# Kernel tuning notes

Hardware: AMD Instinct MI355X
Metric: run time of the kernel (lower is better)

Reference implementation:

```python
import jax, jax.numpy as jnp
import numpy as np
import math

B, H, L = 8, 512, 4096
N2 = 32  # d_state // 2


def setup_inputs() -> dict:
    key = jax.random.key(0)
    ks = jax.random.split(key, 8)
    u = jax.random.normal(ks[0], (B, H, L), dtype=jnp.float32)
    C = jax.random.normal(ks[1], (H, N2, 2), dtype=jnp.float32)  # view_as_real of cfloat C
    # log_dt ~ Uniform[log(dt_min), log(dt_max)], dt_min=1e-3, dt_max=0.1
    log_dt = jax.random.uniform(ks[2], (H,), dtype=jnp.float32,
                                minval=math.log(0.001), maxval=math.log(0.1))
    log_A_real = jnp.log(0.5 * jnp.ones((H, N2), dtype=jnp.float32))
    A_imag = math.pi * jnp.broadcast_to(jnp.arange(N2, dtype=jnp.float32), (H, N2))
    D = jax.random.normal(ks[3], (H,), dtype=jnp.float32)
    # pointwise Conv1d(H, 2H, kernel_size=1): weight (2H, H), bias (2H)
    fan = 1.0 / math.sqrt(H)
    W = jax.random.uniform(ks[4], (2 * H, H), dtype=jnp.float32, minval=-fan, maxval=fan)
    b = jax.random.uniform(ks[5], (2 * H,), dtype=jnp.float32, minval=-fan, maxval=fan)
    return {"u": u, "C": C, "log_dt": log_dt, "log_A_real": log_A_real,
            "A_imag": A_imag, "D": D, "W": W, "b": b}


def reference(u, C, log_dt, log_A_real, A_imag, D, W, b):
    Lb = u.shape[-1]
    # --- S4DKernel: kernel k of shape (H, L) ---
    dt = jnp.exp(log_dt)                                  # (H,)
    Cc = C[..., 0] + 1j * C[..., 1]                       # (H, N2) complex
    A = -jnp.exp(log_A_real) + 1j * A_imag                # (H, N2)
    dtA = A * dt[:, None]                                 # (H, N2)
    # Vandermonde: exp(dtA * l) for l in [0, L)
    K = jnp.exp(dtA[:, :, None] * jnp.arange(Lb, dtype=jnp.float32))  # (H, N2, L)
    Cmod = Cc * (jnp.exp(dtA) - 1.0) / A                  # (H, N2)
    k = 2.0 * jnp.einsum('hn,hnl->hl', Cmod, K).real      # (H, L)
    # --- FFT convolution (length 2L, causal) ---
    n = 2 * Lb
    k_f = jnp.fft.rfft(k, n=n)                            # (H, L+1)
    u_f = jnp.fft.rfft(u, n=n)                            # (B, H, L+1)
    y = jnp.fft.irfft(u_f * k_f, n=n)[..., :Lb]           # (B, H, L)
    # skip connection
    y = y + u * D[:, None]
    # activation (torch nn.GELU default = exact erf form)
    y = jax.nn.gelu(y, approximate=False)
    # pointwise conv (H -> 2H) + GLU over channel dim
    y = jnp.einsum('oh,bhl->bol', W, y) + b[None, :, None]  # (B, 2H, L)
    a, g = jnp.split(y, 2, axis=1)
    return a * jax.nn.sigmoid(g)                          # (B, H, L)
```

## Files before the change

### kernel.cpp

```cpp
#include <hip/hip_runtime.h>
#include <hip/hip_bf16.h>

constexpr int Bn = 8, Hn = 512, Ln = 4096, N2n = 32;

typedef _Float16 f16;
typedef __attribute__((ext_vector_type(8))) _Float16 f16x8;
typedef __attribute__((ext_vector_type(4))) _Float16 f16x4;
typedef __attribute__((ext_vector_type(2))) _Float16 f16x2;
typedef __attribute__((ext_vector_type(4))) float f32x4;

typedef void __attribute__((address_space(1))) gvoid;
typedef void __attribute__((address_space(3))) lvoid;

__global__ __launch_bounds__(64) void k_mats1(
    const float* __restrict__ C, const float* __restrict__ log_dt,
    const float* __restrict__ logA, const float* __restrict__ Aim,
    f16* __restrict__ Vg, f16* __restrict__ A3g, float2* __restrict__ w64g) {
  __shared__ f16 VT[64 * 64];
  __shared__ f16 QT[64 * 64];
  __shared__ float kp[64][33];
  __shared__ float ks[64];
  const int h = blockIdx.x, tid = threadIdx.x, n = tid & 31;

  if (tid < 32) {
    const int idx = h * N2n + n;
    float dt = expf(log_dt[h]);
    float Ar = -expf(logA[idx]);
    float Ai = Aim[idx];
    float dr = Ar * dt, di = Ai * dt;
    float er = expf(dr);
    float wr = er * cosf(di), wi = er * sinf(di);
    float den = Ar * Ar + Ai * Ai;
    float e1r = wr - 1.0f, e1i = wi;
    float tr = (e1r * Ar + e1i * Ai) / den;
    float ti = (e1i * Ar - e1r * Ai) / den;
    float Cr = C[idx * 2 + 0], Ci = C[idx * 2 + 1];
    float c2r = 2.0f * (Cr * tr - Ci * ti);
    float c2i = 2.0f * (Cr * ti + Ci * tr);

    float wpr = 1.f, wpi = 0.f;
    for (int p = 0; p <= 64; ++p) {
      float cwr = c2r * wpr - c2i * wpi;
      float cwi = c2r * wpi + c2i * wpr;
      if (p < 64) {
        const int j = 63 - p, ch = j >> 3, jo = j & 7;
        const int s0 = 2 * n, s1 = 2 * n + 1;
        VT[s0 * 64 + ((ch ^ (s0 & 7)) * 8) + jo] = (f16)wpr;
        VT[s1 * 64 + ((ch ^ (s1 & 7)) * 8) + jo] = (f16)wpi;
        kp[p][n] = cwr;
      }
      if (p >= 1) {
        const int t = p - 1, c0 = 2 * n;
        const int ch = (c0 >> 3) ^ (t & 7);
        QT[t * 64 + ch * 8 + (c0 & 7)]     = (f16)cwr;
        QT[t * 64 + ch * 8 + (c0 & 7) + 1] = (f16)(-cwi);
      }
      if (p == 64) w64g[h * 32 + n] = make_float2(wpr, wpi);
      float nr = wpr * wr - wpi * wi;
      float ni = wpr * wi + wpi * wr;
      wpr = nr; wpi = ni;
    }
  }
  __syncthreads();
  float s = 0.f;
#pragma unroll
  for (int m = 0; m < 32; ++m) s += kp[tid][m];
  ks[tid] = s;
  __syncthreads();
  const int t = tid;
#pragma unroll
  for (int c = 0; c < 8; ++c) {
    f16x8 row;
#pragma unroll
    for (int jo = 0; jo < 8; ++jo) {
      int j = c * 8 + jo;
      row[jo] = (j <= t) ? (f16)ks[t - j] : (f16)0.f;
    }
    *(f16x8*)&A3g[(size_t)h * 8192 + t * 128 + ((c ^ (t & 7)) * 8)] = row;
  }
#pragma unroll
  for (int c = 0; c < 8; ++c)
    *(f16x8*)&Vg[(size_t)h * 4096 + tid * 64 + c * 8] = *(f16x8*)&VT[tid * 64 + c * 8];
#pragma unroll
  for (int c = 0; c < 8; ++c)
    *(f16x8*)&A3g[(size_t)h * 8192 + tid * 128 + 64 + c * 8] = *(f16x8*)&QT[tid * 64 + c * 8];
}

__global__ void conv_w(const float* __restrict__ W, f16* __restrict__ Wh) {
  int i = blockIdx.x * 256 + threadIdx.x;
  if (i < 2 * Hn * Hn) Wh[i] = (f16)W[i];
}

__global__ __launch_bounds__(256, 4) void s4d_mid(
    const float* __restrict__ u, const f16* __restrict__ Vg,
    const f16* __restrict__ A3g, const float2* __restrict__ w64g,
    const float* __restrict__ Dv, f16* __restrict__ yg) {
  __shared__ f16 MATS[8192];
  __shared__ f16 U[4096];
  __shared__ f16 LE[4096];
  __shared__ float2 Pbuf[4][32];
  const int tid = threadIdx.x, wid = tid >> 6, lane = tid & 63;
  const int h = ((blockIdx.x >> 6) << 3) | (blockIdx.x & 7);
  const int b = (blockIdx.x >> 3) & 7;
  const float Dh = Dv[h];

#pragma unroll
  for (int q = 0; q < 2; ++q)
    __builtin_amdgcn_global_load_lds((const gvoid*)(Vg + (size_t)h * 4096 + (q * 256 + tid) * 8),
                                     (lvoid*)&MATS[(q * 256 + wid * 64) * 8], 16, 0, 0);
#pragma unroll
  for (int i = 0; i < 4; ++i) {
    int e = (i * 256 + tid) * 4;
    float4 uv = *(const float4*)(u + ((size_t)(b * Hn + h)) * Ln + e);
    int col = e >> 6, j = e & 63;
    f16x4 hv = {(f16)uv.x, (f16)uv.y, (f16)uv.z, (f16)uv.w};
    *(f16x4*)&U[col * 64 + ((j >> 3) ^ (col & 7)) * 8 + (j & 7)] = hv;
  }
  asm volatile("s_waitcnt vmcnt(0)" ::: "memory");
  __syncthreads();

  const int col = wid * 16 + (lane & 15);
  f32x4 acc[4];
#pragma unroll
  for (int i = 0; i < 4; ++i) acc[i] = (f32x4){0.f, 0.f, 0.f, 0.f};
#pragma unroll
  for (int ks = 0; ks < 2; ++ks) {
    const int kc = ks * 4 + (lane >> 4);
    f16x8 bv = *(const f16x8*)&U[col * 64 + ((kc ^ (col & 7)) * 8)];
#pragma unroll
    for (int mf = 0; mf < 4; ++mf) {
      int row = mf * 16 + (lane & 15);
      f16x8 a = *(const f16x8*)&MATS[row * 64 + ((kc ^ (row & 7)) * 8)];
      acc[mf] = __builtin_amdgcn_mfma_f32_16x16x32_f16(a, bv, acc[mf], 0, 0, 0);
    }
  }
  __syncthreads();

#pragma unroll
  for (int q = 0; q < 4; ++q)
    __builtin_amdgcn_global_load_lds((const gvoid*)(A3g + (size_t)h * 8192 + (q * 256 + tid) * 8),
                                     (lvoid*)&MATS[(q * 256 + wid * 64) * 8], 16, 0, 0);

#pragma unroll
  for (int mf = 0; mf < 4; ++mf) {
    int st0 = mf * 16 + (lane >> 4) * 4;
    f16x4 o = {(f16)acc[mf][0], (f16)acc[mf][1], (f16)acc[mf][2], (f16)acc[mf][3]};
    *(f16x4*)&LE[col * 64 + (((st0 >> 3) ^ (col & 7)) << 3) + (st0 & 7)] = o;
  }
  __syncthreads();

  {
    const int n = lane & 31, q = wid;
    const float2 wT = w64g[h * 32 + n];
    float qr = wT.x, qi = wT.y;
#pragma unroll
    for (int s = 0; s < 4; ++s) {
      float nr = qr * qr - qi * qi;
      float ni = 2.f * qr * qi;
      qr = nr; qi = ni;
    }
    f16x2 Lb[16];
    float er = 0.f, ei = 0.f;
    if (lane < 32) {
#pragma unroll
      for (int k = 0; k < 16; ++k) {
        int blk = q * 16 + k;
        int fi = blk * 64 + (((n >> 2) ^ (blk & 7)) << 3) + ((n & 3) << 1);
        Lb[k] = *(const f16x2*)&LE[fi];
      }
#pragma unroll
      for (int k = 0; k < 16; ++k) {
        float nr = fmaf(wT.x, er, fmaf(-wT.y, ei, (float)Lb[k][0]));
        float ni = fmaf(wT.y, er, fmaf(wT.x, ei, (float)Lb[k][1]));
        er = nr; ei = ni;
      }
      Pbuf[q][n] = make_float2(er, ei);
    }
    __syncthreads();
    if (lane < 32) {
      float orr = 0.f, oii = 0.f;
      for (int p = 0; p < q; ++p) {
        float2 Pp = Pbuf[p][n];
        float nr = fmaf(qr, orr, fmaf(-qi, oii, Pp.x));
        float ni = fmaf(qi, orr, fmaf(qr, oii, Pp.y));
        orr = nr; oii = ni;
      }
      er = orr; ei = oii;
#pragma unroll
      for (int k = 0; k < 16; ++k) {
        int blk = q * 16 + k;
        int fi = blk * 64 + (((n >> 2) ^ (blk & 7)) << 3) + ((n & 3) << 1);
        *(f16x2*)&LE[fi] = (f16x2){(f16)er, (f16)ei};
        float nr = fmaf(wT.x, er, fmaf(-wT.y, ei, (float)Lb[k][0]));
        float ni = fmaf(wT.y, er, fmaf(wT.x, ei, (float)Lb[k][1]));
        er = nr; ei = ni;
      }
    }
  }
  asm volatile("s_waitcnt vmcnt(0)" ::: "memory");
  __syncthreads();

  f32x4 acc4[4];
#pragma unroll
  for (int i = 0; i < 4; ++i) acc4[i] = (f32x4){0.f, 0.f, 0.f, 0.f};
#pragma unroll
  for (int ks = 0; ks < 4; ++ks) {
    const int kc = ks * 4 + (lane >> 4);
    f16x8 bf;
    if (ks < 2) bf = *(const f16x8*)&U[col * 64 + ((kc ^ (col & 7)) << 3)];
    else        bf = *(const f16x8*)&LE[col * 64 + (((kc - 8) ^ (col & 7)) << 3)];
#pragma unroll
    for (int mf = 0; mf < 4; ++mf) {
      int row = mf * 16 + (lane & 15);
      f16x8 af = *(const f16x8*)&MATS[row * 128 + ((kc ^ (row & 7)) << 3)];
      acc4[mf] = __builtin_amdgcn_mfma_f32_16x16x32_f16(af, bf, acc4[mf], 0, 0, 0);
    }
  }
  const int t0 = (lane >> 4) * 4;
#pragma unroll
  for (int mf = 0; mf < 4; ++mf) {
    const int tb = mf * 16 + t0;
    f16x4 uq = *(const f16x4*)&U[col * 64 + (((tb >> 3) ^ (col & 7)) << 3) + (tb & 7)];
    f16x4 o;
#pragma unroll
    for (int r = 0; r < 4; ++r) {
      float v = acc4[mf][r] + Dh * (float)uq[r];
      float g2 = v * fmaf(0.0713548163f, v * v, 1.5957691216f);
      o[r] = (f16)(v * __builtin_amdgcn_rcpf(1.0f + __expf(-g2)));
    }
    *(f16x4*)&yg[((size_t)(b * Hn + h)) * Ln + col * 64 + tb] = o;
  }
}

__global__ __launch_bounds__(256) void k_transpose(
    const f16* __restrict__ yg, f16* __restrict__ gyT) {
  __shared__ float T[64][65];
  const int bid = blockIdx.x, tid = threadIdx.x;
  const int b = bid >> 9, hg = (bid >> 6) & 7, lg = bid & 63;
  const int h0 = hg * 64, l0 = lg * 64;
  const int hi = tid >> 2, lc = (tid & 3) * 16;
  const f16* src = yg + ((size_t)(b * Hn + h0 + hi)) * Ln + l0 + lc;
  f16x8 v0 = *(const f16x8*)src;
  f16x8 v1 = *(const f16x8*)(src + 8);
#pragma unroll
  for (int e = 0; e < 8; ++e) T[lc + e][hi] = (float)v0[e];
#pragma unroll
  for (int e = 0; e < 8; ++e) T[lc + 8 + e][hi] = (float)v1[e];
  __syncthreads();
  const int li = tid >> 2, hc = (tid & 3) * 16;
  f16x8 o0, o1;
#pragma unroll
  for (int e = 0; e < 8; ++e) o0[e] = (f16)T[li][hc + e];
#pragma unroll
  for (int e = 0; e < 8; ++e) o1[e] = (f16)T[li][hc + 8 + e];
  f16* dst = gyT + ((size_t)b * Ln + l0 + li) * Hn + h0 + hc;
  *(f16x8*)dst = o0;
  *(f16x8*)(dst + 8) = o1;
}

__global__ __launch_bounds__(512, 2) void s4d_gemm(
    const f16* __restrict__ Wh, const f16* __restrict__ gyT,
    const float* __restrict__ bias, float* __restrict__ out) {
  __shared__ f16 Asd[2][256 * 64];
  __shared__ f16 Bsd[2][256 * 64];
  __shared__ float biasS[256];
  const int tid = threadIdx.x;
  const int wid = tid >> 6, lane = tid & 63;
  const int nt = blockIdx.x & 127;
  const int mt = blockIdx.x >> 7;
  const int b = nt >> 4;
  const int l0 = (nt & 15) * 256;
  const int m0 = mt * 128;
  const int isG = wid >> 2;
  const int w4 = wid & 3;

  if (tid < 128) biasS[tid] = bias[m0 + tid];
  else if (tid < 256) biasS[tid] = bias[Hn + m0 + (tid - 128)];

  const int srow8 = lane >> 3;
  const int sp = lane & 7;

#define STAGE(BUF, KT)                                                                   \
  {                                                                                      \
    const int k0 = (KT) * 64;                                                            \
    _Pragma("unroll")                                                                    \
    for (int q = 0; q < 4; ++q) {                                                        \
      const int r = q * 64 + wid * 8 + srow8;                                \
      const int wr = (r < 128) ? (m0 + r) : (Hn + m0 + r - 128);                         \
      const f16* srcA = Wh + ((size_t)wr * 512 + k0 + ((sp ^ (r & 7)) * 8));             \
      __builtin_amdgcn_global_load_lds((const gvoid*)srcA,                               \
          (lvoid*)&Asd[BUF][(q * 64 + wid * 8) * 64], 16, 0, 0);                         \
    }                                                                                    \
    _Pragma("unroll")                                                                    \
    for (int q = 0; q < 4; ++q) {                                                        \
      const int r = q * 64 + wid * 8 + srow8;                          \
      const f16* srcB = gyT + (((size_t)b * Ln + l0 + r) * Hn + k0 + ((sp ^ (r & 7)) * 8)); \
      __builtin_amdgcn_global_load_lds((const gvoid*)srcB,                               \
          (lvoid*)&Bsd[BUF][(q * 64 + wid * 8) * 64], 16, 0, 0);                         \
    }                                                                                    \
  }

  f32x4 acc[8][4];
#pragma unroll
  for (int i = 0; i < 8; ++i)
#pragma unroll
    for (int j = 0; j < 4; ++j) acc[i][j] = (f32x4){0.f, 0.f, 0.f, 0.f};

  STAGE(0, 0);
  asm volatile("s_waitcnt vmcnt(0)" ::: "memory");
  __syncthreads();

  for (int kt = 0; kt < 8; ++kt) {
    const int cur = kt & 1;
    if (kt < 7) STAGE(cur ^ 1, kt + 1);
#pragma unroll
    for (int kk = 0; kk < 2; ++kk) {
      const int kc = kk * 4 + (lane >> 4);
      f16x8 bf[4];
#pragma unroll
      for (int nf = 0; nf < 4; ++nf) {
        const int cl = w4 * 64 + nf * 16 + (lane & 15);
        bf[nf] = *(const f16x8*)&Bsd[cur][cl * 64 + ((kc ^ (cl & 7)) * 8)];
      }
#pragma unroll
      for (int mf = 0; mf < 8; ++mf) {
        const int ra = isG * 128 + mf * 16 + (lane & 15);
        f16x8 af = *(const f16x8*)&Asd[cur][ra * 64 + ((kc ^ (ra & 7)) * 8)];
#pragma unroll
        for (int nf = 0; nf < 4; ++nf)
          acc[mf][nf] = __builtin_amdgcn_mfma_f32_16x16x32_f16(af, bf[nf], acc[mf][nf], 0, 0, 0);
      }
    }
    asm volatile("s_waitcnt vmcnt(0)" ::: "memory");
    __syncthreads();
  }

  f16* SIG = &Asd[0][0];
  const int slot = (w4 * 64 + lane) * 128;
  if (isG) {
#pragma unroll
    for (int mf = 0; mf < 8; ++mf) {
#pragma unroll
      for (int np = 0; np < 2; ++np) {
        f16x8 c;
#pragma unroll
        for (int e = 0; e < 8; ++e) {
          const int nf = np * 2 + (e >> 2), r = e & 3;
          const int rowh = mf * 16 + (lane >> 4) * 4 + r;
          float gv = acc[mf][nf][r] + biasS[128 + rowh];
          c[e] = (f16)__builtin_amdgcn_rcpf(1.0f + __expf(-gv));
        }
        const int cid = mf * 2 + np;
        *(f16x8*)&SIG[slot + ((cid ^ (lane & 15)) * 8)] = c;
      }
    }
  }
  __syncthreads();
  if (!isG) {
#pragma unroll
    for (int mf = 0; mf < 8; ++mf) {
#pragma unroll
      for (int np = 0; np < 2; ++np) {
        const int cid = mf * 2 + np;
        f16x8 sg = *(const f16x8*)&SIG[slot + ((cid ^ (lane & 15)) * 8)];
#pragma unroll
        for (int e = 0; e < 8; ++e) {
          const int nf = np * 2 + (e >> 2), r = e & 3;
          const int rowh = mf * 16 + (lane >> 4) * 4 + r;
          const int hh = m0 + rowh;
          const int l = l0 + w4 * 64 + nf * 16 + (lane & 15);
          float av = acc[mf][nf][r] + biasS[rowh];
          out[((size_t)b * Hn + hh) * Ln + l] = av * (float)sg[e];
        }
      }
    }
  }
#undef STAGE
}

extern "C" void kernel_launch(void* const* d_in, const int* in_sizes, int n_in,
                              void* d_out, int out_size, void* d_ws, size_t ws_size,
                              hipStream_t stream) {
  (void)in_sizes; (void)n_in; (void)out_size; (void)ws_size;
  const float* u     = (const float*)d_in[0];
  const float* C     = (const float*)d_in[1];
  const float* logdt = (const float*)d_in[2];
  const float* logA  = (const float*)d_in[3];
  const float* Aim   = (const float*)d_in[4];
  const float* Dv    = (const float*)d_in[5];
  const float* W     = (const float*)d_in[6];
  const float* bias  = (const float*)d_in[7];
  float* out = (float*)d_out;

  char* ws = (char*)d_ws;
  f16*    gyT  = (f16*)ws;
  f16*    Vg   = (f16*)(ws + (size_t)(32 << 20));
  f16*    A3g  = (f16*)(ws + (size_t)(36 << 20));
  float2* w64g = (float2*)(ws + (size_t)(44 << 20));
  f16*    Wh   = (f16*)(ws + (size_t)(45 << 20));
  f16*    yg   = (f16*)d_out;

  hipLaunchKernelGGL(k_mats1, dim3(Hn), dim3(64), 0, stream, C, logdt, logA, Aim, Vg, A3g, w64g);
  hipLaunchKernelGGL(conv_w, dim3(2048), dim3(256), 0, stream, W, Wh);
  hipLaunchKernelGGL(s4d_mid, dim3(Hn * Bn), dim3(256), 0, stream, u, Vg, A3g, w64g, Dv, yg);
  hipLaunchKernelGGL(k_transpose, dim3(Bn * 8 * 64), dim3(256), 0, stream, yg, gyT);
  hipLaunchKernelGGL(s4d_gemm, dim3(512), dim3(512), 0, stream, Wh, gyT, bias, out);
}
```

Baseline: 103.1 us.

## Pre-swizzle W into MFMA fragment order and load A operands directly

The weight conversion kernel now writes W in f16 already arranged in MFMA A-fragment order, using vectorized 8-wide stores. The GEMM drops the A shared-memory tile and has each lane load its fragments straight from global memory with contiguous 16-byte reads. This halves the LDS footprint and removes A staging and LDS reads, which could raise occupancy. The cost is that A loads are no longer prefetched through the double buffer, so global latency may show up in the inner loop.

After: 114.7 us. +11.3%, slower.

```diff
diff --git a/kernel.cpp b/kernel.cpp
--- a/kernel.cpp
+++ b/kernel.cpp
@@ -86,9 +86,21 @@
     *(f16x8*)&A3g[(size_t)h * 8192 + tid * 128 + 64 + c * 8] = *(f16x8*)&QT[tid * 64 + c * 8];
 }
 
-__global__ void conv_w(const float* __restrict__ W, f16* __restrict__ Wh) {
-  int i = blockIdx.x * 256 + threadIdx.x;
-  if (i < 2 * Hn * Hn) Wh[i] = (f16)W[i];
+__global__ void conv_w(const float* __restrict__ W, f16* __restrict__ WhF) {
+  int g = blockIdx.x * 256 + threadIdx.x;
+  int lane = g & 63;
+  int mf = (g >> 6) & 7;
+  int kk = (g >> 9) & 1;
+  int kt = (g >> 10) & 7;
+  int mt = (g >> 13) & 3;
+  int isG = (g >> 15) & 1;
+  int wr = isG * 512 + mt * 128 + mf * 16 + (lane & 15);
+  int k  = kt * 64 + kk * 32 + (lane >> 4) * 8;
+  const float4* src = (const float4*)(W + (size_t)wr * 512 + k);
+  float4 a = src[0], c = src[1];
+  f16x8 o = {(f16)a.x, (f16)a.y, (f16)a.z, (f16)a.w,
+             (f16)c.x, (f16)c.y, (f16)c.z, (f16)c.w};
+  *(f16x8*)&WhF[(size_t)g * 8] = o;
 }
 
 __global__ __launch_bounds__(256, 4) void s4d_mid(
@@ -259,9 +271,8 @@
 }
 
 __global__ __launch_bounds__(512, 2) void s4d_gemm(
-    const f16* __restrict__ Wh, const f16* __restrict__ gyT,
+    const f16* __restrict__ WhF, const f16* __restrict__ gyT,
     const float* __restrict__ bias, float* __restrict__ out) {
-  __shared__ f16 Asd[2][256 * 64];
   __shared__ f16 Bsd[2][256 * 64];
   __shared__ float biasS[256];
   const int tid = threadIdx.x;
@@ -280,24 +291,16 @@
   const int srow8 = lane >> 3;
   const int sp = lane & 7;
 
-#define STAGE(BUF, KT)                                                                   \
-  {                                                                                      \
-    const int k0 = (KT) * 64;                                                            \
-    _Pragma("unroll")                                                                    \
-    for (int q = 0; q < 4; ++q) {                                                        \
-      const int r = q * 64 + wid * 8 + srow8;                                \
-      const int wr = (r < 128) ? (m0 + r) : (Hn + m0 + r - 128);                         \
-      const f16* srcA = Wh + ((size_t)wr * 512 + k0 + ((sp ^ (r & 7)) * 8));             \
-      __builtin_amdgcn_global_load_lds((const gvoid*)srcA,                               \
-          (lvoid*)&Asd[BUF][(q * 64 + wid * 8) * 64], 16, 0, 0);                         \
-    }                                                                                    \
-    _Pragma("unroll")                                                                    \
-    for (int q = 0; q < 4; ++q) {                                                        \
-      const int r = q * 64 + wid * 8 + srow8;                          \
+#define STAGE_B(BUF, KT)                                                                   \
+  {                                                                                        \
+    const int k0 = (KT) * 64;                                                              \
+    _Pragma("unroll")                                                                      \
+    for (int q = 0; q < 4; ++q) {                                                          \
+      const int r = q * 64 + wid * 8 + srow8;                            \
       const f16* srcB = gyT + (((size_t)b * Ln + l0 + r) * Hn + k0 + ((sp ^ (r & 7)) * 8)); \
-      __builtin_amdgcn_global_load_lds((const gvoid*)srcB,                               \
-          (lvoid*)&Bsd[BUF][(q * 64 + wid * 8) * 64], 16, 0, 0);                         \
-    }                                                                                    \
+      __builtin_amdgcn_global_load_lds((const gvoid*)srcB,                                 \
+          (lvoid*)&Bsd[BUF][(q * 64 + wid * 8) * 64], 16, 0, 0);                           \
+    }                                                                                      \
   }
 
   f32x4 acc[8][4];
@@ -306,13 +309,21 @@
 #pragma unroll
     for (int j = 0; j < 4; ++j) acc[i][j] = (f32x4){0.f, 0.f, 0.f, 0.f};
 
-  STAGE(0, 0);
+  const f16* Abase = WhF + (size_t)(isG * 4 + mt) * (8 * 2 * 8 * 512) + lane * 8;
+
+  STAGE_B(0, 0);
   asm volatile("s_waitcnt vmcnt(0)" ::: "memory");
   __syncthreads();
 
   for (int kt = 0; kt < 8; ++kt) {
     const int cur = kt & 1;
-    if (kt < 7) STAGE(cur ^ 1, kt + 1);
+    if (kt < 7) STAGE_B(cur ^ 1, kt + 1);
+    const f16* At = Abase + (size_t)kt * (2 * 8 * 512);
+    f16x8 afA[8], afB[8];
+#pragma unroll
+    for (int mf = 0; mf < 8; ++mf) afA[mf] = *(const f16x8*)(At + mf * 512);
+#pragma unroll
+    for (int mf = 0; mf < 8; ++mf) afB[mf] = *(const f16x8*)(At + (8 + mf) * 512);
 #pragma unroll
     for (int kk = 0; kk < 2; ++kk) {
       const int kc = kk * 4 + (lane >> 4);
@@ -324,8 +335,7 @@
       }
 #pragma unroll
       for (int mf = 0; mf < 8; ++mf) {
-        const int ra = isG * 128 + mf * 16 + (lane & 15);
-        f16x8 af = *(const f16x8*)&Asd[cur][ra * 64 + ((kc ^ (ra & 7)) * 8)];
+        const f16x8 af = kk ? afB[mf] : afA[mf];
 #pragma unroll
         for (int nf = 0; nf < 4; ++nf)
           acc[mf][nf] = __builtin_amdgcn_mfma_f32_16x16x32_f16(af, bf[nf], acc[mf][nf], 0, 0, 0);
@@ -335,7 +345,7 @@
     __syncthreads();
   }
 
-  f16* SIG = &Asd[0][0];
+  f16* SIG = &Bsd[0][0];
   const int slot = (w4 * 64 + lane) * 128;
   if (isG) {
 #pragma unroll
@@ -375,7 +385,7 @@
       }
     }
   }
-#undef STAGE
+#undef STAGE_B
 }
 
 extern "C" void kernel_launch(void* const* d_in, const int* in_sizes, int n_in,
@@ -397,12 +407,12 @@
   f16*    Vg   = (f16*)(ws + (size_t)(32 << 20));
   f16*    A3g  = (f16*)(ws + (size_t)(36 << 20));
   float2* w64g = (float2*)(ws + (size_t)(44 << 20));
-  f16*    Wh   = (f16*)(ws + (size_t)(45 << 20));
+  f16*    WhF  = (f16*)(ws + (size_t)(45 << 20));
   f16*    yg   = (f16*)d_out;
 
   hipLaunchKernelGGL(k_mats1, dim3(Hn), dim3(64), 0, stream, C, logdt, logA, Aim, Vg, A3g, w64g);
-  hipLaunchKernelGGL(conv_w, dim3(2048), dim3(256), 0, stream, W, Wh);
+  hipLaunchKernelGGL(conv_w, dim3(256), dim3(256), 0, stream, W, WhF);
   hipLaunchKernelGGL(s4d_mid, dim3(Hn * Bn), dim3(256), 0, stream, u, Vg, A3g, w64g, Dv, yg);
   hipLaunchKernelGGL(k_transpose, dim3(Bn * 8 * 64), dim3(256), 0, stream, yg, gyT);
-  hipLaunchKernelGGL(s4d_gemm, dim3(512), dim3(512), 0, stream, Wh, gyT, bias, out);
-}
+  hipLaunchKernelGGL(s4d_gemm, dim3(512), dim3(512), 0, stream, WhF, gyT, bias, out);
+}
```
